# Kernel optimization log

Measured on AMD Instinct MI355X. Metric: run time of the kernel, lower is better.

Reference implementation:

```python
import jax, jax.numpy as jnp
import numpy as np

B, T, I, U, BB = 256, 1024, 64, 128, 256


def lecun_tanh(x):
    return 1.7159 * jnp.tanh(0.666 * x)


def _linear_init(key, fan_in, fan_out):
    # torch nn.Linear default: U(-1/sqrt(fan_in), 1/sqrt(fan_in)) for weight and bias
    kw, kb = jax.random.split(key)
    lim = 1.0 / np.sqrt(fan_in)
    W = jax.random.uniform(kw, (fan_in, fan_out), jnp.float32, -lim, lim)
    b = jax.random.uniform(kb, (fan_out,), jnp.float32, -lim, lim)
    return W, b


def setup_inputs() -> dict:
    key = jax.random.key(0)
    ks = jax.random.split(key, 6)
    x = jax.random.normal(ks[0], (B, T, I), jnp.float32)
    W_bb, b_bb = _linear_init(ks[1], I + U, BB)
    W_ff1, b_ff1 = _linear_init(ks[2], BB, U)
    W_ff2, b_ff2 = _linear_init(ks[3], BB, U)
    W_ta, b_ta = _linear_init(ks[4], BB, U)
    W_tb, b_tb = _linear_init(ks[5], BB, U)
    return {
        "x": x,
        "W_bb": W_bb, "b_bb": b_bb,
        "W_ff1": W_ff1, "b_ff1": b_ff1,
        "W_ff2": W_ff2, "b_ff2": b_ff2,
        "W_ta": W_ta, "b_ta": b_ta,
        "W_tb": W_tb, "b_tb": b_tb,
    }


def reference(x, W_bb, b_bb, W_ff1, b_ff1, W_ff2, b_ff2, W_ta, b_ta, W_tb, b_tb):
    # CfC, non-wired, mode='default', activation='lecun_tanh', backbone_layers=1,
    # mixed_memory=False, proj_size=None (fc = Identity), timespans=None (ts = 1.0).
    ts = jnp.float32(1.0)

    def step(h, xt):
        z = jnp.concatenate([xt, h], axis=-1)            # [B, I+U]
        z = lecun_tanh(z @ W_bb + b_bb)                   # backbone, [B, BB]
        ff1 = jnp.tanh(z @ W_ff1 + b_ff1)                 # [B, U]
        ff2 = jnp.tanh(z @ W_ff2 + b_ff2)                 # [B, U]
        t_a = z @ W_ta + b_ta
        t_b = z @ W_tb + b_tb
        t_interp = jax.nn.sigmoid(t_a * ts + t_b)
        h_new = ff1 * (1.0 - t_interp) + t_interp * ff2
        return h_new, h_new

    h0 = jnp.zeros((x.shape[0], W_ff1.shape[1]), x.dtype)
    h_last, ys = jax.lax.scan(step, h0, jnp.swapaxes(x, 0, 1))  # scan over T
    readout = jnp.swapaxes(ys, 0, 1)                      # [B, T, U]
    return readout, h_last
```

## Files before the change

### kernel.cpp

```cpp
#include <hip/hip_runtime.h>


typedef __bf16 bf16;
typedef __bf16 bf16x8 __attribute__((ext_vector_type(8)));
typedef float  f32x4  __attribute__((ext_vector_type(4)));

#define BDIM 512

constexpr int B_  = 256;
constexpr int T_  = 1024;
constexpr int I_  = 64;
constexpr int U_  = 128;
constexpr int BB_ = 256;
constexpr int ROWS = 16;
constexpr int NBLK = B_ / ROWS;
constexpr int KO1  = (I_ + U_) / 8;

__device__ __forceinline__ float tanh_fast(float x) {
  float e = __builtin_amdgcn_exp2f(x * 2.8853900817779268f);
  return 1.0f - 2.0f * __builtin_amdgcn_rcpf(e + 1.0f);
}
__device__ __forceinline__ float sigmoid_fast(float x) {
  return __builtin_amdgcn_rcpf(1.0f + __builtin_amdgcn_exp2f(x * -1.4426950408889634f));
}

__device__ __forceinline__ void barrier_lds() {
  asm volatile("s_waitcnt lgkmcnt(0)" ::: "memory");
  __builtin_amdgcn_s_barrier();
}

__global__ __launch_bounds__(BDIM, 2)
void cfc_kernel(const float* __restrict__ x,
                const float* __restrict__ Wbb,  const float* __restrict__ bbb,
                const float* __restrict__ Wff1, const float* __restrict__ bff1,
                const float* __restrict__ Wff2, const float* __restrict__ bff2,
                const float* __restrict__ Wta,  const float* __restrict__ bta,
                const float* __restrict__ Wtb,  const float* __restrict__ btb,
                float* __restrict__ out)
{
  __shared__ __align__(16) bf16 Abuf[KO1 * ROWS * 8];
  __shared__ __align__(16) bf16 Zbuf[32  * ROWS * 8];

  const int tid  = threadIdx.x;
  const int w    = tid >> 6;
  const int l    = tid & 63;
  const int quad = l >> 4;
  const int l16  = l & 15;
  const int bg   = blockIdx.x;

  const int c1 = w * 32 + l16;
  const int u  = w * 16 + l16;

  bf16x8 f1[6][2];
  #pragma unroll
  for (int ks = 0; ks < 6; ks++)
    #pragma unroll
    for (int nt = 0; nt < 2; nt++)
      #pragma unroll
      for (int j = 0; j < 8; j++) {
        int k = ks * 32 + quad * 8 + j;
        f1[ks][nt][j] = (bf16)Wbb[k * BB_ + c1 + nt * 16];
      }

  bf16x8 g2[8][3];
  #pragma unroll
  for (int r = 0; r < 8; r++) {
    int ks = (w + r) & 7;
    #pragma unroll
    for (int j = 0; j < 8; j++) {
      int k = ks * 32 + quad * 8 + j;
      g2[r][0][j] = (bf16)Wff1[k * U_ + u];
      g2[r][1][j] = (bf16)Wff2[k * U_ + u];
      g2[r][2][j] = (bf16)(Wta[k * U_ + u] + Wtb[k * U_ + u]);
    }
  }

  const float bz0 = bbb[c1];
  const float bz1 = bbb[c1 + 16];
  const float bh0 = bff1[u];
  const float bh1 = bff2[u];
  const float bh2 = bta[u] + btb[u];

  for (int idx = tid; idx < (KO1 - 8) * ROWS * 8; idx += BDIM)
    Abuf[8 * ROWS * 8 + idx] = (bf16)0.0f;

  const int xm  = tid >> 5;
  const int xkk = tid & 31;
  const float* xsrc = x + ((size_t)(bg * ROWS + xm) * T_) * I_ + 2 * xkk;
  bf16* xdst = &Abuf[(((2 * xkk) >> 3) * ROWS + xm) * 8 + ((2 * xkk) & 7)];

  {
    float2 v = *(const float2*)xsrc;
    xdst[0] = (bf16)v.x;
    xdst[1] = (bf16)v.y;
  }
  __syncthreads();

  float* outp  = out + (size_t)(bg * ROWS) * T_ * U_ + u;
  float* hlast = out + (size_t)B_ * T_ * U_ + (size_t)(bg * ROWS) * U_ + u;

  const int h_oct = (64 + u) >> 3;
  const int h_sub = (64 + u) & 7;

  float hreg[4];

  float2 xv_cur = *(const float2*)(xsrc + I_);

  for (int t = 0; t < T_; ++t) {
    if (t) {
      #pragma unroll
      for (int i = 0; i < 4; i++)
        outp[(size_t)(quad * 4 + i) * T_ * U_ + (size_t)(t - 1) * U_] = hreg[i];
    }

    f32x4 az0 = { bz0, bz0, bz0, bz0 };
    f32x4 az1 = { bz1, bz1, bz1, bz1 };
    #pragma unroll
    for (int ks = 0; ks < 6; ks++) {
      bf16x8 a = *(const bf16x8*)&Abuf[((ks * 4 + quad) * ROWS + l16) * 8];
      az0 = __builtin_amdgcn_mfma_f32_16x16x32_bf16(a, f1[ks][0], az0, 0, 0, 0);
      az1 = __builtin_amdgcn_mfma_f32_16x16x32_bf16(a, f1[ks][1], az1, 0, 0, 0);
    }
    #pragma unroll
    for (int i = 0; i < 4; i++) {
      int m = quad * 4 + i;
      float z0 = 1.7159f * tanh_fast(0.666f * az0[i]);
      float z1 = 1.7159f * tanh_fast(0.666f * az1[i]);
      int c0 = c1, cB = c1 + 16;
      Zbuf[((c0 >> 3) * ROWS + m) * 8 + (c0 & 7)] = (bf16)z0;
      Zbuf[((cB >> 3) * ROWS + m) * 8 + (cB & 7)] = (bf16)z1;
    }

    f32x4 a0 = { bh0, bh0, bh0, bh0 };
    f32x4 a1 = { bh1, bh1, bh1, bh1 };
    f32x4 a2 = { bh2, bh2, bh2, bh2 };

    {
      bf16x8 zf0 = *(const bf16x8*)&Zbuf[((w * 4 + quad) * ROWS + l16) * 8];
      a0 = __builtin_amdgcn_mfma_f32_16x16x32_bf16(zf0, g2[0][0], a0, 0, 0, 0);
      a1 = __builtin_amdgcn_mfma_f32_16x16x32_bf16(zf0, g2[0][1], a1, 0, 0, 0);
      a2 = __builtin_amdgcn_mfma_f32_16x16x32_bf16(zf0, g2[0][2], a2, 0, 0, 0);
    }
    barrier_lds();

    bf16x8 zf[7];
    #pragma unroll
    for (int r = 1; r < 8; r++) {
      const int ks = (w + r) & 7;
      zf[r - 1] = *(const bf16x8*)&Zbuf[((ks * 4 + quad) * ROWS + l16) * 8];
    }

    xdst[0] = (bf16)xv_cur.x;
    xdst[1] = (bf16)xv_cur.y;
    {
      const int tn = (t + 2 < T_) ? (t + 2) : (T_ - 1);
      xv_cur = *(const float2*)(xsrc + (size_t)tn * I_);
    }

    #pragma unroll
    for (int r = 1; r < 8; r++) {
      a0 = __builtin_amdgcn_mfma_f32_16x16x32_bf16(zf[r - 1], g2[r][0], a0, 0, 0, 0);
      a1 = __builtin_amdgcn_mfma_f32_16x16x32_bf16(zf[r - 1], g2[r][1], a1, 0, 0, 0);
    }
    #pragma unroll
    for (int r = 1; r < 8; r++)
      a2 = __builtin_amdgcn_mfma_f32_16x16x32_bf16(zf[r - 1], g2[r][2], a2, 0, 0, 0);

    float ff1v[4], ff2v[4];
    #pragma unroll
    for (int i = 0; i < 4; i++) ff1v[i] = tanh_fast(a0[i]);
    #pragma unroll
    for (int i = 0; i < 4; i++) ff2v[i] = tanh_fast(a1[i]);

    #pragma unroll
    for (int i = 0; i < 4; i++) {
      int m = quad * 4 + i;
      float s = sigmoid_fast(a2[i]);
      float h = ff1v[i] + s * (ff2v[i] - ff1v[i]);
      hreg[i] = h;
      Abuf[(h_oct * ROWS + m) * 8 + h_sub] = (bf16)h;
    }

    barrier_lds();
  }

  #pragma unroll
  for (int i = 0; i < 4; i++) {
    outp[(size_t)(quad * 4 + i) * T_ * U_ + (size_t)(T_ - 1) * U_] = hreg[i];
    hlast[(size_t)(quad * 4 + i) * U_] = hreg[i];
  }
}

extern "C" void kernel_launch(void* const* d_in, const int* in_sizes, int n_in,
                              void* d_out, int out_size, void* d_ws, size_t ws_size,
                              hipStream_t stream) {
  const float* x    = (const float*)d_in[0];
  const float* Wbb  = (const float*)d_in[1];
  const float* bbb  = (const float*)d_in[2];
  const float* Wff1 = (const float*)d_in[3];
  const float* bff1 = (const float*)d_in[4];
  const float* Wff2 = (const float*)d_in[5];
  const float* bff2 = (const float*)d_in[6];
  const float* Wta  = (const float*)d_in[7];
  const float* bta  = (const float*)d_in[8];
  const float* Wtb  = (const float*)d_in[9];
  const float* btb  = (const float*)d_in[10];
  float* out = (float*)d_out;
  (void)in_sizes; (void)n_in; (void)out_size; (void)d_ws; (void)ws_size;

  hipLaunchKernelGGL(cfc_kernel, dim3(NBLK), dim3(BDIM), 0, stream,
                     x, Wbb, bbb, Wff1, bff1, Wff2, bff2, Wta, bta, Wtb, btb, out);
}
```

Before: 1.563 ms.

## Halve block to four waves, each computing twice the output columns

After: 2.662 ms. 1.7x slower.

```diff
diff --git a/kernel.cpp b/kernel.cpp
--- a/kernel.cpp
+++ b/kernel.cpp
@@ -5,7 +5,7 @@
 typedef __bf16 bf16x8 __attribute__((ext_vector_type(8)));
 typedef float  f32x4  __attribute__((ext_vector_type(4)));
 
-#define BDIM 512
+#define BDIM 256
 
 constexpr int B_  = 256;
 constexpr int T_  = 1024;
@@ -29,7 +29,7 @@
   __builtin_amdgcn_s_barrier();
 }
 
-__global__ __launch_bounds__(BDIM, 2)
+__global__ __launch_bounds__(BDIM, 1)
 void cfc_kernel(const float* __restrict__ x,
                 const float* __restrict__ Wbb,  const float* __restrict__ bbb,
                 const float* __restrict__ Wff1, const float* __restrict__ bff1,
@@ -48,147 +48,169 @@
   const int l16  = l & 15;
   const int bg   = blockIdx.x;
 
-  const int c1 = w * 32 + l16;
-  const int u  = w * 16 + l16;
-
-  bf16x8 f1[6][2];
+  const int c1 = w * 64 + l16;
+  const int u0 = w * 32 + l16;
+
+  bf16x8 f1[6][4];
   #pragma unroll
   for (int ks = 0; ks < 6; ks++)
     #pragma unroll
-    for (int nt = 0; nt < 2; nt++)
+    for (int nt = 0; nt < 4; nt++)
       #pragma unroll
       for (int j = 0; j < 8; j++) {
         int k = ks * 32 + quad * 8 + j;
         f1[ks][nt][j] = (bf16)Wbb[k * BB_ + c1 + nt * 16];
       }
 
-  bf16x8 g2[8][3];
+  bf16x8 g2[8][2][3];
   #pragma unroll
   for (int r = 0; r < 8; r++) {
-    int ks = (w + r) & 7;
-    #pragma unroll
-    for (int j = 0; j < 8; j++) {
-      int k = ks * 32 + quad * 8 + j;
-      g2[r][0][j] = (bf16)Wff1[k * U_ + u];
-      g2[r][1][j] = (bf16)Wff2[k * U_ + u];
-      g2[r][2][j] = (bf16)(Wta[k * U_ + u] + Wtb[k * U_ + u]);
-    }
-  }
-
-  const float bz0 = bbb[c1];
-  const float bz1 = bbb[c1 + 16];
-  const float bh0 = bff1[u];
-  const float bh1 = bff2[u];
-  const float bh2 = bta[u] + btb[u];
+    int ks = (2 * w + r) & 7;
+    #pragma unroll
+    for (int nt = 0; nt < 2; nt++)
+      #pragma unroll
+      for (int j = 0; j < 8; j++) {
+        int k = ks * 32 + quad * 8 + j;
+        int u = u0 + nt * 16;
+        g2[r][nt][0][j] = (bf16)Wff1[k * U_ + u];
+        g2[r][nt][1][j] = (bf16)Wff2[k * U_ + u];
+        g2[r][nt][2][j] = (bf16)(Wta[k * U_ + u] + Wtb[k * U_ + u]);
+      }
+  }
+
+  float bz[4], bh[2][3];
+  #pragma unroll
+  for (int nt = 0; nt < 4; nt++) bz[nt] = bbb[c1 + nt * 16];
+  #pragma unroll
+  for (int nt = 0; nt < 2; nt++) {
+    bh[nt][0] = bff1[u0 + nt * 16];
+    bh[nt][1] = bff2[u0 + nt * 16];
+    bh[nt][2] = bta[u0 + nt * 16] + btb[u0 + nt * 16];
+  }
 
   for (int idx = tid; idx < (KO1 - 8) * ROWS * 8; idx += BDIM)
     Abuf[8 * ROWS * 8 + idx] = (bf16)0.0f;
 
-  const int xm  = tid >> 5;
-  const int xkk = tid & 31;
-  const float* xsrc = x + ((size_t)(bg * ROWS + xm) * T_) * I_ + 2 * xkk;
-  bf16* xdst = &Abuf[(((2 * xkk) >> 3) * ROWS + xm) * 8 + ((2 * xkk) & 7)];
+  const int xm  = tid >> 4;
+  const int xk  = (tid & 15) * 4;
+  const float* xsrc = x + ((size_t)(bg * ROWS + xm) * T_) * I_ + xk;
+  bf16* xdst = &Abuf[((xk >> 3) * ROWS + xm) * 8 + (xk & 7)];
 
   {
-    float2 v = *(const float2*)xsrc;
-    xdst[0] = (bf16)v.x;
-    xdst[1] = (bf16)v.y;
+    float4 v = *(const float4*)xsrc;
+    xdst[0] = (bf16)v.x; xdst[1] = (bf16)v.y;
+    xdst[2] = (bf16)v.z; xdst[3] = (bf16)v.w;
   }
   __syncthreads();
 
-  float* outp  = out + (size_t)(bg * ROWS) * T_ * U_ + u;
-  float* hlast = out + (size_t)B_ * T_ * U_ + (size_t)(bg * ROWS) * U_ + u;
-
-  const int h_oct = (64 + u) >> 3;
-  const int h_sub = (64 + u) & 7;
-
-  float hreg[4];
-
-  float2 xv_cur = *(const float2*)(xsrc + I_);
+  float* outp  = out + (size_t)(bg * ROWS) * T_ * U_ + u0;
+  float* hlast = out + (size_t)B_ * T_ * U_ + (size_t)(bg * ROWS) * U_ + u0;
+
+  const int h_oct = (64 + u0) >> 3;
+  const int h_sub = (64 + u0) & 7;
+
+  float hreg[2][4];
+
+  float4 xv_cur = *(const float4*)(xsrc + I_);
 
   for (int t = 0; t < T_; ++t) {
     if (t) {
       #pragma unroll
-      for (int i = 0; i < 4; i++)
-        outp[(size_t)(quad * 4 + i) * T_ * U_ + (size_t)(t - 1) * U_] = hreg[i];
-    }
-
-    f32x4 az0 = { bz0, bz0, bz0, bz0 };
-    f32x4 az1 = { bz1, bz1, bz1, bz1 };
+      for (int nt = 0; nt < 2; nt++)
+        #pragma unroll
+        for (int i = 0; i < 4; i++)
+          outp[(size_t)(quad * 4 + i) * T_ * U_ + (size_t)(t - 1) * U_ + nt * 16] = hreg[nt][i];
+    }
+
+    f32x4 az[4];
+    #pragma unroll
+    for (int nt = 0; nt < 4; nt++) az[nt] = f32x4{ bz[nt], bz[nt], bz[nt], bz[nt] };
     #pragma unroll
     for (int ks = 0; ks < 6; ks++) {
       bf16x8 a = *(const bf16x8*)&Abuf[((ks * 4 + quad) * ROWS + l16) * 8];
-      az0 = __builtin_amdgcn_mfma_f32_16x16x32_bf16(a, f1[ks][0], az0, 0, 0, 0);
-      az1 = __builtin_amdgcn_mfma_f32_16x16x32_bf16(a, f1[ks][1], az1, 0, 0, 0);
-    }
-    #pragma unroll
-    for (int i = 0; i < 4; i++) {
-      int m = quad * 4 + i;
-      float z0 = 1.7159f * tanh_fast(0.666f * az0[i]);
-      float z1 = 1.7159f * tanh_fast(0.666f * az1[i]);
-      int c0 = c1, cB = c1 + 16;
-      Zbuf[((c0 >> 3) * ROWS + m) * 8 + (c0 & 7)] = (bf16)z0;
-      Zbuf[((cB >> 3) * ROWS + m) * 8 + (cB & 7)] = (bf16)z1;
-    }
-
-    f32x4 a0 = { bh0, bh0, bh0, bh0 };
-    f32x4 a1 = { bh1, bh1, bh1, bh1 };
-    f32x4 a2 = { bh2, bh2, bh2, bh2 };
-
-    {
-      bf16x8 zf0 = *(const bf16x8*)&Zbuf[((w * 4 + quad) * ROWS + l16) * 8];
-      a0 = __builtin_amdgcn_mfma_f32_16x16x32_bf16(zf0, g2[0][0], a0, 0, 0, 0);
-      a1 = __builtin_amdgcn_mfma_f32_16x16x32_bf16(zf0, g2[0][1], a1, 0, 0, 0);
-      a2 = __builtin_amdgcn_mfma_f32_16x16x32_bf16(zf0, g2[0][2], a2, 0, 0, 0);
+      #pragma unroll
+      for (int nt = 0; nt < 4; nt++)
+        az[nt] = __builtin_amdgcn_mfma_f32_16x16x32_bf16(a, f1[ks][nt], az[nt], 0, 0, 0);
+    }
+    #pragma unroll
+    for (int nt = 0; nt < 4; nt++)
+      #pragma unroll
+      for (int i = 0; i < 4; i++) {
+        int m = quad * 4 + i;
+        int c = c1 + nt * 16;
+        float zv = 1.7159f * tanh_fast(0.666f * az[nt][i]);
+        Zbuf[((c >> 3) * ROWS + m) * 8 + (c & 7)] = (bf16)zv;
+      }
+
+    f32x4 acc[2][3];
+    #pragma unroll
+    for (int nt = 0; nt < 2; nt++)
+      #pragma unroll
+      for (int o = 0; o < 3; o++)
+        acc[nt][o] = f32x4{ bh[nt][o], bh[nt][o], bh[nt][o], bh[nt][o] };
+
+    #pragma unroll
+    for (int r = 0; r < 2; r++) {
+      const int ks = (2 * w + r) & 7;
+      bf16x8 zf0 = *(const bf16x8*)&Zbuf[((ks * 4 + quad) * ROWS + l16) * 8];
+      #pragma unroll
+      for (int nt = 0; nt < 2; nt++)
+        #pragma unroll
+        for (int o = 0; o < 3; o++)
+          acc[nt][o] = __builtin_amdgcn_mfma_f32_16x16x32_bf16(zf0, g2[r][nt][o], acc[nt][o], 0, 0, 0);
     }
     barrier_lds();
 
-    bf16x8 zf[7];
-    #pragma unroll
-    for (int r = 1; r < 8; r++) {
-      const int ks = (w + r) & 7;
-      zf[r - 1] = *(const bf16x8*)&Zbuf[((ks * 4 + quad) * ROWS + l16) * 8];
-    }
-
-    xdst[0] = (bf16)xv_cur.x;
-    xdst[1] = (bf16)xv_cur.y;
+    bf16x8 zf[6];
+    #pragma unroll
+    for (int r = 2; r < 8; r++) {
+      const int ks = (2 * w + r) & 7;
+      zf[r - 2] = *(const bf16x8*)&Zbuf[((ks * 4 + quad) * ROWS + l16) * 8];
+    }
+
+    xdst[0] = (bf16)xv_cur.x; xdst[1] = (bf16)xv_cur.y;
+    xdst[2] = (bf16)xv_cur.z; xdst[3] = (bf16)xv_cur.w;
     {
       const int tn = (t + 2 < T_) ? (t + 2) : (T_ - 1);
-      xv_cur = *(const float2*)(xsrc + (size_t)tn * I_);
-    }
-
-    #pragma unroll
-    for (int r = 1; r < 8; r++) {
-      a0 = __builtin_amdgcn_mfma_f32_16x16x32_bf16(zf[r - 1], g2[r][0], a0, 0, 0, 0);
-      a1 = __builtin_amdgcn_mfma_f32_16x16x32_bf16(zf[r - 1], g2[r][1], a1, 0, 0, 0);
-    }
-    #pragma unroll
-    for (int r = 1; r < 8; r++)
-      a2 = __builtin_amdgcn_mfma_f32_16x16x32_bf16(zf[r - 1], g2[r][2], a2, 0, 0, 0);
-
-    float ff1v[4], ff2v[4];
-    #pragma unroll
-    for (int i = 0; i < 4; i++) ff1v[i] = tanh_fast(a0[i]);
-    #pragma unroll
-    for (int i = 0; i < 4; i++) ff2v[i] = tanh_fast(a1[i]);
-
+      xv_cur = *(const float4*)(xsrc + (size_t)tn * I_);
+    }
+
+    #pragma unroll
+    for (int r = 2; r < 8; r++) {
+      #pragma unroll
+      for (int nt = 0; nt < 2; nt++)
+        #pragma unroll
+        for (int o = 0; o < 3; o++)
+          acc[nt][o] = __builtin_amdgcn_mfma_f32_16x16x32_bf16(zf[r - 2], g2[r][nt][o], acc[nt][o], 0, 0, 0);
+    }
+
+    #pragma unroll
+    for (int nt = 0; nt < 2; nt++) {
+      float ff1v[4], ff2v[4];
+      #pragma unroll
+      for (int i = 0; i < 4; i++) ff1v[i] = tanh_fast(acc[nt][0][i]);
+      #pragma unroll
+      for (int i = 0; i < 4; i++) ff2v[i] = tanh_fast(acc[nt][1][i]);
+      #pragma unroll
+      for (int i = 0; i < 4; i++) {
+        int m = quad * 4 + i;
+        float s = sigmoid_fast(acc[nt][2][i]);
+        float h = ff1v[i] + s * (ff2v[i] - ff1v[i]);
+        hreg[nt][i] = h;
+        Abuf[((h_oct + nt * 2) * ROWS + m) * 8 + h_sub] = (bf16)h;
+      }
+    }
+
+    barrier_lds();
+  }
+
+  #pragma unroll
+  for (int nt = 0; nt < 2; nt++)
     #pragma unroll
     for (int i = 0; i < 4; i++) {
-      int m = quad * 4 + i;
-      float s = sigmoid_fast(a2[i]);
-      float h = ff1v[i] + s * (ff2v[i] - ff1v[i]);
-      hreg[i] = h;
-      Abuf[(h_oct * ROWS + m) * 8 + h_sub] = (bf16)h;
-    }
-
-    barrier_lds();
-  }
-
-  #pragma unroll
-  for (int i = 0; i < 4; i++) {
-    outp[(size_t)(quad * 4 + i) * T_ * U_ + (size_t)(T_ - 1) * U_] = hreg[i];
-    hlast[(size_t)(quad * 4 + i) * U_] = hreg[i];
-  }
+      outp[(size_t)(quad * 4 + i) * T_ * U_ + (size_t)(T_ - 1) * U_ + nt * 16] = hreg[nt][i];
+      hlast[(size_t)(quad * 4 + i) * U_ + nt * 16] = hreg[nt][i];
+    }
 }
 
 extern "C" void kernel_launch(void* const* d_in, const int* in_sizes, int n_in,
```

## Precompute input projection x@W_bb in a parallel kernel before the recurrence

Applied to the files above, without the earlier changes.

Result: no change. 1.548 ms (-0.9%).

```diff
diff --git a/kernel.cpp b/kernel.cpp
--- a/kernel.cpp
+++ b/kernel.cpp
@@ -29,17 +29,73 @@
   __builtin_amdgcn_s_barrier();
 }
 
+__global__ __launch_bounds__(512, 2)
+void xz_precompute(const float* __restrict__ x,
+                   const float* __restrict__ Wbb,
+                   const float* __restrict__ bbb,
+                   float4* __restrict__ ws)
+{
+  const int tid  = threadIdx.x;
+  const int w    = tid >> 6;
+  const int l    = tid & 63;
+  const int quad = l >> 4;
+  const int l16  = l & 15;
+  const int bg   = blockIdx.x >> 4;
+  const int t0   = (blockIdx.x & 15) * 64;
+
+  const int c1 = w * 32 + l16;
+
+  bf16x8 fx[2][2];
+  #pragma unroll
+  for (int ks = 0; ks < 2; ks++)
+    #pragma unroll
+    for (int nt = 0; nt < 2; nt++)
+      #pragma unroll
+      for (int j = 0; j < 8; j++)
+        fx[ks][nt][j] = (bf16)Wbb[(ks * 32 + quad * 8 + j) * BB_ + c1 + nt * 16];
+
+  const float bz0 = bbb[c1];
+  const float bz1 = bbb[c1 + 16];
+
+  const float* xs = x + ((size_t)(bg * ROWS + l16) * T_) * I_ + quad * 8;
+
+  for (int t = t0; t < t0 + 64; ++t) {
+    const float* xt = xs + (size_t)t * I_;
+    float4 a0lo = *(const float4*)(xt);
+    float4 a0hi = *(const float4*)(xt + 4);
+    float4 a1lo = *(const float4*)(xt + 32);
+    float4 a1hi = *(const float4*)(xt + 36);
+
+    bf16x8 af[2];
+    af[0][0]=(bf16)a0lo.x; af[0][1]=(bf16)a0lo.y; af[0][2]=(bf16)a0lo.z; af[0][3]=(bf16)a0lo.w;
+    af[0][4]=(bf16)a0hi.x; af[0][5]=(bf16)a0hi.y; af[0][6]=(bf16)a0hi.z; af[0][7]=(bf16)a0hi.w;
+    af[1][0]=(bf16)a1lo.x; af[1][1]=(bf16)a1lo.y; af[1][2]=(bf16)a1lo.z; af[1][3]=(bf16)a1lo.w;
+    af[1][4]=(bf16)a1hi.x; af[1][5]=(bf16)a1hi.y; af[1][6]=(bf16)a1hi.z; af[1][7]=(bf16)a1hi.w;
+
+    f32x4 az0 = { bz0, bz0, bz0, bz0 };
+    f32x4 az1 = { bz1, bz1, bz1, bz1 };
+    #pragma unroll
+    for (int ks = 0; ks < 2; ks++) {
+      az0 = __builtin_amdgcn_mfma_f32_16x16x32_bf16(af[ks], fx[ks][0], az0, 0, 0, 0);
+      az1 = __builtin_amdgcn_mfma_f32_16x16x32_bf16(af[ks], fx[ks][1], az1, 0, 0, 0);
+    }
+    size_t base = ((size_t)((bg * T_ + t) * 8 + w) * 2) * 64 + l;
+    ws[base]      = *(const float4*)&az0;
+    ws[base + 64] = *(const float4*)&az1;
+  }
+}
+
 __global__ __launch_bounds__(BDIM, 2)
-void cfc_kernel(const float* __restrict__ x,
-                const float* __restrict__ Wbb,  const float* __restrict__ bbb,
-                const float* __restrict__ Wff1, const float* __restrict__ bff1,
-                const float* __restrict__ Wff2, const float* __restrict__ bff2,
-                const float* __restrict__ Wta,  const float* __restrict__ bta,
-                const float* __restrict__ Wtb,  const float* __restrict__ btb,
-                float* __restrict__ out)
+void cfc_kernel_ws(const float* __restrict__ Wbb,
+                   const float* __restrict__ Wff1, const float* __restrict__ bff1,
+                   const float* __restrict__ Wff2, const float* __restrict__ bff2,
+                   const float* __restrict__ Wta,  const float* __restrict__ bta,
+                   const float* __restrict__ Wtb,  const float* __restrict__ btb,
+                   const float4* __restrict__ ws,
+                   float* __restrict__ out)
 {
-  __shared__ __align__(16) bf16 Abuf[KO1 * ROWS * 8];
-  __shared__ __align__(16) bf16 Zbuf[32  * ROWS * 8];
+  __shared__ __align__(16) bf16 Abuf[16 * ROWS * 8];
+  __shared__ __align__(16) bf16 Zbuf[32 * ROWS * 8];
 
   const int tid  = threadIdx.x;
   const int w    = tid >> 6;
@@ -51,15 +107,15 @@
   const int c1 = w * 32 + l16;
   const int u  = w * 16 + l16;
 
-  bf16x8 f1[6][2];
-  #pragma unroll
-  for (int ks = 0; ks < 6; ks++)
+  bf16x8 f1h[4][2];
+  #pragma unroll
+  for (int ks = 0; ks < 4; ks++)
     #pragma unroll
     for (int nt = 0; nt < 2; nt++)
       #pragma unroll
       for (int j = 0; j < 8; j++) {
-        int k = ks * 32 + quad * 8 + j;
-        f1[ks][nt][j] = (bf16)Wbb[k * BB_ + c1 + nt * 16];
+        int k = 64 + ks * 32 + quad * 8 + j;
+        f1h[ks][nt][j] = (bf16)Wbb[k * BB_ + c1 + nt * 16];
       }
 
   bf16x8 g2[8][3];
@@ -75,36 +131,25 @@
     }
   }
 
-  const float bz0 = bbb[c1];
-  const float bz1 = bbb[c1 + 16];
   const float bh0 = bff1[u];
   const float bh1 = bff2[u];
   const float bh2 = bta[u] + btb[u];
 
-  for (int idx = tid; idx < (KO1 - 8) * ROWS * 8; idx += BDIM)
-    Abuf[8 * ROWS * 8 + idx] = (bf16)0.0f;
-
-  const int xm  = tid >> 5;
-  const int xkk = tid & 31;
-  const float* xsrc = x + ((size_t)(bg * ROWS + xm) * T_) * I_ + 2 * xkk;
-  bf16* xdst = &Abuf[(((2 * xkk) >> 3) * ROWS + xm) * 8 + ((2 * xkk) & 7)];
-
-  {
-    float2 v = *(const float2*)xsrc;
-    xdst[0] = (bf16)v.x;
-    xdst[1] = (bf16)v.y;
-  }
+  for (int idx = tid; idx < 16 * ROWS * 8; idx += BDIM)
+    Abuf[idx] = (bf16)0.0f;
   __syncthreads();
 
   float* outp  = out + (size_t)(bg * ROWS) * T_ * U_ + u;
   float* hlast = out + (size_t)B_ * T_ * U_ + (size_t)(bg * ROWS) * U_ + u;
 
-  const int h_oct = (64 + u) >> 3;
-  const int h_sub = (64 + u) & 7;
+  const int h_oct = u >> 3;
+  const int h_sub = u & 7;
 
   float hreg[4];
 
-  float2 xv_cur = *(const float2*)(xsrc + I_);
+  const float4* wsp = ws + ((size_t)(bg * T_) * 8 + w) * 2 * 64 + l;
+  float4 xz0 = wsp[0];
+  float4 xz1 = wsp[64];
 
   for (int t = 0; t < T_; ++t) {
     if (t) {
@@ -113,13 +158,13 @@
         outp[(size_t)(quad * 4 + i) * T_ * U_ + (size_t)(t - 1) * U_] = hreg[i];
     }
 
-    f32x4 az0 = { bz0, bz0, bz0, bz0 };
-    f32x4 az1 = { bz1, bz1, bz1, bz1 };
-    #pragma unroll
-    for (int ks = 0; ks < 6; ks++) {
+    f32x4 az0 = *(const f32x4*)&xz0;
+    f32x4 az1 = *(const f32x4*)&xz1;
+    #pragma unroll
+    for (int ks = 0; ks < 4; ks++) {
       bf16x8 a = *(const bf16x8*)&Abuf[((ks * 4 + quad) * ROWS + l16) * 8];
-      az0 = __builtin_amdgcn_mfma_f32_16x16x32_bf16(a, f1[ks][0], az0, 0, 0, 0);
-      az1 = __builtin_amdgcn_mfma_f32_16x16x32_bf16(a, f1[ks][1], az1, 0, 0, 0);
+      az0 = __builtin_amdgcn_mfma_f32_16x16x32_bf16(a, f1h[ks][0], az0, 0, 0, 0);
+      az1 = __builtin_amdgcn_mfma_f32_16x16x32_bf16(a, f1h[ks][1], az1, 0, 0, 0);
     }
     #pragma unroll
     for (int i = 0; i < 4; i++) {
@@ -134,7 +179,166 @@
     f32x4 a0 = { bh0, bh0, bh0, bh0 };
     f32x4 a1 = { bh1, bh1, bh1, bh1 };
     f32x4 a2 = { bh2, bh2, bh2, bh2 };
-
+    {
+      bf16x8 zf0 = *(const bf16x8*)&Zbuf[((w * 4 + quad) * ROWS + l16) * 8];
+      a0 = __builtin_amdgcn_mfma_f32_16x16x32_bf16(zf0, g2[0][0], a0, 0, 0, 0);
+      a1 = __builtin_amdgcn_mfma_f32_16x16x32_bf16(zf0, g2[0][1], a1, 0, 0, 0);
+      a2 = __builtin_amdgcn_mfma_f32_16x16x32_bf16(zf0, g2[0][2], a2, 0, 0, 0);
+    }
+    barrier_lds();
+
+    bf16x8 zf[7];
+    #pragma unroll
+    for (int r = 1; r < 8; r++) {
+      const int ks = (w + r) & 7;
+      zf[r - 1] = *(const bf16x8*)&Zbuf[((ks * 4 + quad) * ROWS + l16) * 8];
+    }
+
+    {
+      const int tn = (t + 1 < T_) ? (t + 1) : (T_ - 1);
+      const float4* p = wsp + (size_t)tn * (8 * 2 * 64);
+      xz0 = p[0];
+      xz1 = p[64];
+    }
+
+    #pragma unroll
+    for (int r = 1; r < 8; r++) {
+      a0 = __builtin_amdgcn_mfma_f32_16x16x32_bf16(zf[r - 1], g2[r][0], a0, 0, 0, 0);
+      a1 = __builtin_amdgcn_mfma_f32_16x16x32_bf16(zf[r - 1], g2[r][1], a1, 0, 0, 0);
+    }
+    #pragma unroll
+    for (int r = 1; r < 8; r++)
+      a2 = __builtin_amdgcn_mfma_f32_16x16x32_bf16(zf[r - 1], g2[r][2], a2, 0, 0, 0);
+
+    float ff1v[4], ff2v[4];
+    #pragma unroll
+    for (int i = 0; i < 4; i++) ff1v[i] = tanh_fast(a0[i]);
+    #pragma unroll
+    for (int i = 0; i < 4; i++) ff2v[i] = tanh_fast(a1[i]);
+
+    #pragma unroll
+    for (int i = 0; i < 4; i++) {
+      int m = quad * 4 + i;
+      float s = sigmoid_fast(a2[i]);
+      float h = ff1v[i] + s * (ff2v[i] - ff1v[i]);
+      hreg[i] = h;
+      Abuf[(h_oct * ROWS + m) * 8 + h_sub] = (bf16)h;
+    }
+
+    barrier_lds();
+  }
+
+  #pragma unroll
+  for (int i = 0; i < 4; i++) {
+    outp[(size_t)(quad * 4 + i) * T_ * U_ + (size_t)(T_ - 1) * U_] = hreg[i];
+    hlast[(size_t)(quad * 4 + i) * U_] = hreg[i];
+  }
+}
+
+__global__ __launch_bounds__(BDIM, 2)
+void cfc_kernel_fb(const float* __restrict__ x,
+                   const float* __restrict__ Wbb,  const float* __restrict__ bbb,
+                   const float* __restrict__ Wff1, const float* __restrict__ bff1,
+                   const float* __restrict__ Wff2, const float* __restrict__ bff2,
+                   const float* __restrict__ Wta,  const float* __restrict__ bta,
+                   const float* __restrict__ Wtb,  const float* __restrict__ btb,
+                   float* __restrict__ out)
+{
+  __shared__ __align__(16) bf16 Abuf[KO1 * ROWS * 8];
+  __shared__ __align__(16) bf16 Zbuf[32  * ROWS * 8];
+
+  const int tid  = threadIdx.x;
+  const int w    = tid >> 6;
+  const int l    = tid & 63;
+  const int quad = l >> 4;
+  const int l16  = l & 15;
+  const int bg   = blockIdx.x;
+
+  const int c1 = w * 32 + l16;
+  const int u  = w * 16 + l16;
+
+  bf16x8 f1[6][2];
+  #pragma unroll
+  for (int ks = 0; ks < 6; ks++)
+    #pragma unroll
+    for (int nt = 0; nt < 2; nt++)
+      #pragma unroll
+      for (int j = 0; j < 8; j++) {
+        int k = ks * 32 + quad * 8 + j;
+        f1[ks][nt][j] = (bf16)Wbb[k * BB_ + c1 + nt * 16];
+      }
+
+  bf16x8 g2[8][3];
+  #pragma unroll
+  for (int r = 0; r < 8; r++) {
+    int ks = (w + r) & 7;
+    #pragma unroll
+    for (int j = 0; j < 8; j++) {
+      int k = ks * 32 + quad * 8 + j;
+      g2[r][0][j] = (bf16)Wff1[k * U_ + u];
+      g2[r][1][j] = (bf16)Wff2[k * U_ + u];
+      g2[r][2][j] = (bf16)(Wta[k * U_ + u] + Wtb[k * U_ + u]);
+    }
+  }
+
+  const float bz0 = bbb[c1];
+  const float bz1 = bbb[c1 + 16];
+  const float bh0 = bff1[u];
+  const float bh1 = bff2[u];
+  const float bh2 = bta[u] + btb[u];
+
+  for (int idx = tid; idx < (KO1 - 8) * ROWS * 8; idx += BDIM)
+    Abuf[8 * ROWS * 8 + idx] = (bf16)0.0f;
+
+  const int xm  = tid >> 5;
+  const int xkk = tid & 31;
+  const float* xsrc = x + ((size_t)(bg * ROWS + xm) * T_) * I_ + 2 * xkk;
+  bf16* xdst = &Abuf[(((2 * xkk) >> 3) * ROWS + xm) * 8 + ((2 * xkk) & 7)];
+
+  {
+    float2 v = *(const float2*)xsrc;
+    xdst[0] = (bf16)v.x;
+    xdst[1] = (bf16)v.y;
+  }
+  __syncthreads();
+
+  float* outp  = out + (size_t)(bg * ROWS) * T_ * U_ + u;
+  float* hlast = out + (size_t)B_ * T_ * U_ + (size_t)(bg * ROWS) * U_ + u;
+
+  const int h_oct = (64 + u) >> 3;
+  const int h_sub = (64 + u) & 7;
+
+  float hreg[4];
+  float2 xv_cur = *(const float2*)(xsrc + I_);
+
+  for (int t = 0; t < T_; ++t) {
+    if (t) {
+      #pragma unroll
+      for (int i = 0; i < 4; i++)
+        outp[(size_t)(quad * 4 + i) * T_ * U_ + (size_t)(t - 1) * U_] = hreg[i];
+    }
+
+    f32x4 az0 = { bz0, bz0, bz0, bz0 };
+    f32x4 az1 = { bz1, bz1, bz1, bz1 };
+    #pragma unroll
+    for (int ks = 0; ks < 6; ks++) {
+      bf16x8 a = *(const bf16x8*)&Abuf[((ks * 4 + quad) * ROWS + l16) * 8];
+      az0 = __builtin_amdgcn_mfma_f32_16x16x32_bf16(a, f1[ks][0], az0, 0, 0, 0);
+      az1 = __builtin_amdgcn_mfma_f32_16x16x32_bf16(a, f1[ks][1], az1, 0, 0, 0);
+    }
+    #pragma unroll
+    for (int i = 0; i < 4; i++) {
+      int m = quad * 4 + i;
+      float z0 = 1.7159f * tanh_fast(0.666f * az0[i]);
+      float z1 = 1.7159f * tanh_fast(0.666f * az1[i]);
+      int c0 = c1, cB = c1 + 16;
+      Zbuf[((c0 >> 3) * ROWS + m) * 8 + (c0 & 7)] = (bf16)z0;
+      Zbuf[((cB >> 3) * ROWS + m) * 8 + (cB & 7)] = (bf16)z1;
+    }
+
+    f32x4 a0 = { bh0, bh0, bh0, bh0 };
+    f32x4 a1 = { bh1, bh1, bh1, bh1 };
+    f32x4 a2 = { bh2, bh2, bh2, bh2 };
     {
       bf16x8 zf0 = *(const bf16x8*)&Zbuf[((w * 4 + quad) * ROWS + l16) * 8];
       a0 = __builtin_amdgcn_mfma_f32_16x16x32_bf16(zf0, g2[0][0], a0, 0, 0, 0);
@@ -206,8 +410,19 @@
   const float* Wtb  = (const float*)d_in[9];
   const float* btb  = (const float*)d_in[10];
   float* out = (float*)d_out;
-  (void)in_sizes; (void)n_in; (void)out_size; (void)d_ws; (void)ws_size;
-
-  hipLaunchKernelGGL(cfc_kernel, dim3(NBLK), dim3(BDIM), 0, stream,
-                     x, Wbb, bbb, Wff1, bff1, Wff2, bff2, Wta, bta, Wtb, btb, out);
-}
+  (void)in_sizes; (void)n_in; (void)out_size;
+
+  const size_t need = (size_t)NBLK * T_ * 8 * 2 * 64 * sizeof(float4);
+
+  if (d_ws != nullptr && ws_size >= need) {
+    float4* ws = (float4*)d_ws;
+    hipLaunchKernelGGL(xz_precompute, dim3(256), dim3(512), 0, stream,
+                       x, Wbb, bbb, ws);
+    hipLaunchKernelGGL(cfc_kernel_ws, dim3(NBLK), dim3(BDIM), 0, stream,
+                       Wbb, Wff1, bff1, Wff2, bff2, Wta, bta, Wtb, btb,
+                       (const float4*)ws, out);
+  } else {
+    hipLaunchKernelGGL(cfc_kernel_fb, dim3(NBLK), dim3(BDIM), 0, stream,
+                       x, Wbb, bbb, Wff1, bff1, Wff2, bff2, Wta, bta, Wtb, btb, out);
+  }
+}
```
